# Optimization experiments

Hardware: AMD Instinct MI355X
Metric: run time of the kernel (lower is better)

The kernel has to match this reference:

```python
import jax, jax.numpy as jnp
import numpy as np

EPS = 1e-5


def layer_norm(x, g, b):
    mu = jnp.mean(x, axis=-1, keepdims=True)
    var = jnp.var(x, axis=-1, keepdims=True)
    return (x - mu) * jax.lax.rsqrt(var + EPS) * g + b


def setup_inputs() -> dict:
    key = jax.random.key(0)
    ks = jax.random.split(key, 10)
    B, N, D, H, DFF = 4, 2048, 384, 6, 2048
    s = lambda fan: 1.0 / np.sqrt(fan)
    return {
        "x": jax.random.normal(ks[0], (B, N, D), dtype=jnp.float32),
        "norm_g": jnp.ones((D,), jnp.float32),
        "norm_b": jnp.zeros((D,), jnp.float32),
        "w_qkv": jax.random.uniform(ks[1], (D, 3 * D), jnp.float32, -s(D), s(D)),
        "b_qkv": jax.random.uniform(ks[2], (3 * D,), jnp.float32, -s(D), s(D)),
        "w1": jax.random.uniform(ks[3], (D, DFF), jnp.float32, -s(D), s(D)),
        "b1": jax.random.uniform(ks[4], (DFF,), jnp.float32, -s(D), s(D)),
        "w2": jax.random.uniform(ks[5], (DFF, D), jnp.float32, -s(DFF), s(DFF)),
        "b2": jax.random.uniform(ks[6], (D,), jnp.float32, -s(DFF), s(DFF)),
    }


def reference(x, norm_g, norm_b, w_qkv, b_qkv, w1, b1, w2, b2):
    H = 6
    B, N, D = x.shape
    hd = D // H
    scale = hd ** -0.5

    # --- attention (pre-norm, shared LayerNorm params) ---
    out = layer_norm(x, norm_g, norm_b)
    qkv = out @ w_qkv + b_qkv                     # [B, N, 3D]
    q, k, v = jnp.split(qkv, 3, axis=-1)
    to_heads = lambda t: t.reshape(B, N, H, hd).transpose(0, 2, 1, 3)  # b h n d
    q, k, v = to_heads(q), to_heads(k), to_heads(v)
    scores = jnp.einsum('bhid,bhjd->bhij', q, k) * scale
    attn = jax.nn.softmax(scores, axis=-1)        # dropout is identity in eval
    att = jnp.einsum('bhij,bhjd->bhid', attn, v)  # [B, H, N, hd]
    att = att.transpose(0, 2, 1, 3).reshape(B, N, D)
    x2 = x + att

    # --- MLP (same shared LayerNorm) ---
    y = layer_norm(x2, norm_g, norm_b)
    h = jax.nn.gelu(y @ w1 + b1, approximate=False)  # torch F.gelu exact
    mlp = h @ w2 + b2
    return x2 + mlp
```

## Files before the change

kernel.cpp:

```cpp
#include <hip/hip_runtime.h>
#include <cstdint>
#include <cstddef>

#define DEV static __device__ __forceinline__

typedef __attribute__((ext_vector_type(8))) short short8;
typedef __attribute__((ext_vector_type(16))) float f32x16;
typedef __attribute__((ext_vector_type(4))) unsigned short u16x4;
typedef __attribute__((ext_vector_type(2))) unsigned short u16x2;

constexpr int kB = 4, kN = 2048, kD = 384, kH = 6, kDFF = 2048;
constexpr int kM = kB * kN;
constexpr int kBH = kB * kH;
constexpr float kQPre = 0.18033688011112042f;

DEV float exp2fast(float f) { return __builtin_amdgcn_exp2f(f); }

DEV unsigned short f2b(float f) {
  union { float fp; uint32_t u; } v; v.fp = f;
  return (unsigned short)((v.u + 0x7fffu + ((v.u >> 16) & 1u)) >> 16);
}

DEV void gload16(const unsigned short* g, unsigned short* l) {
  __builtin_amdgcn_global_load_lds(
      (const __attribute__((address_space(1))) unsigned int*)g,
      (__attribute__((address_space(3))) unsigned int*)l, 16, 0, 0);
}

DEV float gelu_fast(float x) {
  float t = exp2fast(x * (2.3022081f + 0.1029432f * x * x));
  return x - x * __builtin_amdgcn_rcpf(t + 1.0f);
}

__global__ __launch_bounds__(256) void k_pre(
    const float* __restrict__ wqkv, unsigned short* __restrict__ wqkvT,
    const float* __restrict__ w1,   unsigned short* __restrict__ w1T,
    const float* __restrict__ w2,   unsigned short* __restrict__ w2T,
    const float* __restrict__ x, const float* __restrict__ g,
    const float* __restrict__ bta, unsigned short* __restrict__ y) {
  const int tid = threadIdx.x;
  if (blockIdx.x >= 492) {
    int row  = (blockIdx.x - 492) * 4 + (tid >> 6);
    int lane = tid & 63;
    const float* xr = x + (size_t)row * kD;
    float4 a = *(const float4*)(xr + lane * 4);
    float2 c = *(const float2*)(xr + 256 + lane * 2);
    float s  = a.x + a.y + a.z + a.w + c.x + c.y;
    float ss = a.x*a.x + a.y*a.y + a.z*a.z + a.w*a.w + c.x*c.x + c.y*c.y;
#pragma unroll
    for (int m = 1; m < 64; m <<= 1) {
      s  += __shfl_xor(s,  m, 64);
      ss += __shfl_xor(ss, m, 64);
    }
    float mean = s * (1.0f / kD);
    float var  = ss * (1.0f / kD) - mean * mean;
    float r = rsqrtf(var + 1e-5f);
    float4 g4 = *(const float4*)(g + lane * 4);
    float2 g2 = *(const float2*)(g + 256 + lane * 2);
    float4 b4 = *(const float4*)(bta + lane * 4);
    float2 b2 = *(const float2*)(bta + 256 + lane * 2);
    unsigned short* yr = y + (size_t)row * kD;
    u16x4 o4;
    o4[0] = f2b((a.x - mean) * r * g4.x + b4.x);
    o4[1] = f2b((a.y - mean) * r * g4.y + b4.y);
    o4[2] = f2b((a.z - mean) * r * g4.z + b4.z);
    o4[3] = f2b((a.w - mean) * r * g4.w + b4.w);
    *(u16x4*)(yr + lane * 4) = o4;
    u16x2 o2;
    o2[0] = f2b((c.x - mean) * r * g2.x + b2.x);
    o2[1] = f2b((c.y - mean) * r * g2.y + b2.y);
    *(u16x2*)(yr + 256 + lane * 2) = o2;
    return;
  }
  __shared__ unsigned short t[64][66];
  int idx = blockIdx.x;
  const float* w; unsigned short* wT; int K, Nn, nbk;
  if (idx < 108)      { w = wqkv; wT = wqkvT; K = 384;  Nn = 1152; nbk = 6; }
  else if (idx < 300) { w = w1;   wT = w1T;   K = 384;  Nn = 2048; nbk = 6;  idx -= 108; }
  else                { w = w2;   wT = w2T;   K = 2048; Nn = 384;  nbk = 32; idx -= 300; }
  const int bk = idx % nbk, bn = idx / nbk;
  const int k0 = bk << 6, n0 = bn << 6;
  const int cl = tid & 63, rw = tid >> 6;
#pragma unroll
  for (int it = 0; it < 16; ++it) {
    int kk = it * 4 + rw;
    t[cl][kk] = f2b(w[(size_t)(k0 + kk) * Nn + n0 + cl]);
  }
  __syncthreads();
  const int kq = (tid & 15) << 2;
  const int nr = tid >> 4;
#pragma unroll
  for (int it = 0; it < 4; ++it) {
    int nn = it * 16 + nr;
    u16x4 v;
    v[0] = t[nn][kq]; v[1] = t[nn][kq + 1]; v[2] = t[nn][kq + 2]; v[3] = t[nn][kq + 3];
    *(u16x4*)&wT[(size_t)(n0 + nn) * K + k0 + kq] = v;
  }
}

__global__ __launch_bounds__(256) void k_layernorm(
    const float* __restrict__ x, const float* __restrict__ g,
    const float* __restrict__ bta, unsigned short* __restrict__ y) {
  int row  = blockIdx.x * 4 + (threadIdx.x >> 6);
  int lane = threadIdx.x & 63;
  const float* xr = x + (size_t)row * kD;
  float4 a = *(const float4*)(xr + lane * 4);
  float2 c = *(const float2*)(xr + 256 + lane * 2);
  float s  = a.x + a.y + a.z + a.w + c.x + c.y;
  float ss = a.x*a.x + a.y*a.y + a.z*a.z + a.w*a.w + c.x*c.x + c.y*c.y;
#pragma unroll
  for (int m = 1; m < 64; m <<= 1) {
    s  += __shfl_xor(s,  m, 64);
    ss += __shfl_xor(ss, m, 64);
  }
  float mean = s * (1.0f / kD);
  float var  = ss * (1.0f / kD) - mean * mean;
  float r = rsqrtf(var + 1e-5f);
  float4 g4 = *(const float4*)(g + lane * 4);
  float2 g2 = *(const float2*)(g + 256 + lane * 2);
  float4 b4 = *(const float4*)(bta + lane * 4);
  float2 b2 = *(const float2*)(bta + 256 + lane * 2);
  unsigned short* yr = y + (size_t)row * kD;
  u16x4 o4;
  o4[0] = f2b((a.x - mean) * r * g4.x + b4.x);
  o4[1] = f2b((a.y - mean) * r * g4.y + b4.y);
  o4[2] = f2b((a.z - mean) * r * g4.z + b4.z);
  o4[3] = f2b((a.w - mean) * r * g4.w + b4.w);
  *(u16x4*)(yr + lane * 4) = o4;
  u16x2 o2;
  o2[0] = f2b((c.x - mean) * r * g2.x + b2.x);
  o2[1] = f2b((c.y - mean) * r * g2.y + b2.y);
  *(u16x2*)(yr + 256 + lane * 2) = o2;
}

template <int MODE, int TM>
__global__ __launch_bounds__(256) void k_gemm(
    const unsigned short* __restrict__ A, const unsigned short* __restrict__ Bt,
    const float* __restrict__ bias, int K, int Nn, int nbm,
    unsigned short* __restrict__ oq, unsigned short* __restrict__ okk,
    unsigned short* __restrict__ ov, unsigned short* __restrict__ oh,
    const float* __restrict__ res, float* __restrict__ out) {
  constexpr int FI = (TM >= 64) ? TM / 64 : 1;
  constexpr int FJ = (TM >= 64) ? 2 : 1;
  __shared__ unsigned short lA[2][TM * 32];
  __shared__ unsigned short lB[2][128 * 32];
  const int tid = threadIdx.x, wid = tid >> 6, lane = tid & 63;
  const int bm = blockIdx.x % nbm, bn = blockIdx.x / nbm;
  const int m0 = bm * TM, n0 = bn * 128;
  const int wr = (TM >= 64) ? (wid >> 1) : 0;
  const int wc = (TM >= 64) ? (wid & 1) : wid;
  const int wmo = wr * (TM >> 1);
  const int wno = wc * (FJ * 32);
  const int l31 = lane & 31, lh = lane >> 5;
  const int gsw = (l31 >> 1) & 3;

  f32x16 acc[FI][FJ];
#pragma unroll
  for (int i = 0; i < FI; i++)
#pragma unroll
    for (int j = 0; j < FJ; j++)
#pragma unroll
      for (int r = 0; r < 16; r++) acc[i][j][r] = 0.f;

  const int srow = (lane >> 2);
  const int scc  = (lane & 3) << 3;

  auto stage = [&](int buf, int k0) {
    if constexpr (TM >= 64) {
#pragma unroll
      for (int p = 0; p < TM / 64; p++) {
        int row = ((wid + (p << 2)) << 4) + srow;
        int sl  = ((lane & 3) ^ ((row >> 1) & 3)) << 3;
        gload16(A + (size_t)(m0 + row) * K + k0 + sl, &lA[buf][(row << 5) + scc]);
      }
    } else {
      if (tid < TM * 4) {
        int row = tid >> 2;
        int sl  = ((tid & 3) ^ ((row >> 1) & 3)) << 3;
        gload16(A + (size_t)(m0 + row) * K + k0 + sl,
                &lA[buf][(row << 5) + ((tid & 3) << 3)]);
      }
    }
#pragma unroll
    for (int p = 0; p < 2; p++) {
      int row = ((wid + (p << 2)) << 4) + srow;
      int sl  = ((lane & 3) ^ ((row >> 1) & 3)) << 3;
      gload16(Bt + (size_t)(n0 + row) * K + k0 + sl, &lB[buf][(row << 5) + scc]);
    }
  };

  stage(0, 0);

  const int nkt = K >> 5;
  for (int kt = 0; kt < nkt; ++kt) {
    const int cur = kt & 1;
    __syncthreads();
    if (kt + 1 < nkt) stage(cur ^ 1, (kt + 1) << 5);
    short8 af[FI][2], bf[FJ][2];
#pragma unroll
    for (int i = 0; i < FI; i++)
#pragma unroll
      for (int ks = 0; ks < 2; ks++)
        af[i][ks] = *(const short8*)&lA[cur][(wmo + (i << 5) + l31) * 32 +
                                            ((((ks << 1) + lh) ^ gsw) << 3)];
#pragma unroll
    for (int j = 0; j < FJ; j++)
#pragma unroll
      for (int ks = 0; ks < 2; ks++)
        bf[j][ks] = *(const short8*)&lB[cur][(wno + (j << 5) + l31) * 32 +
                                            ((((ks << 1) + lh) ^ gsw) << 3)];
#pragma unroll
    for (int i = 0; i < FI; i++)
#pragma unroll
      for (int j = 0; j < FJ; j++)
#pragma unroll
        for (int ks = 0; ks < 2; ks++)
          acc[i][j] = __builtin_amdgcn_mfma_f32_32x32x16_bf16(af[i][ks], bf[j][ks],
                                                              acc[i][j], 0, 0, 0);
  }

#pragma unroll
  for (int i = 0; i < FI; i++) {
#pragma unroll
    for (int j = 0; j < FJ; j++) {
      int col = n0 + wno + (j << 5) + l31;
      float bv = bias[col];
#pragma unroll
      for (int reg = 0; reg < 16; ++reg) {
        int m = m0 + wmo + (i << 5) + (reg & 3) + ((reg >> 2) << 3) + (lh << 2);
        float cvl = acc[i][j][reg] + bv;
        if (MODE == 0) {
          int bI = m >> 11, nI = m & 2047;
          if (col < 384) {
            int hh = col >> 6, dd = col & 63;
            oq[(((size_t)bI * kH + hh) * kN + nI) * 64 + dd] = f2b(cvl * kQPre);
          } else if (col < 768) {
            int c2 = col - 384; int hh = c2 >> 6, dd = c2 & 63;
            okk[(((size_t)bI * kH + hh) * kN + nI) * 64 + dd] = f2b(cvl);
          } else {
            int c2 = col - 768; int hh = c2 >> 6, dd = c2 & 63;
            ov[(((size_t)bI * kH + hh) * 64 + dd) * kN + nI] = f2b(cvl);
          }
        } else if (MODE == 1) {
          oh[(size_t)m * kDFF + col] = f2b(gelu_fast(cvl));
        } else {
          size_t idx = (size_t)m * kD + col;
          out[idx] = res[idx] + cvl;
        }
      }
    }
  }
}

__global__ __launch_bounds__(256) void k_attn(
    const unsigned short* __restrict__ Q, const unsigned short* __restrict__ Kg,
    const unsigned short* __restrict__ Vt, const float* __restrict__ x,
    float* __restrict__ x2) {
  __shared__ unsigned short sh[4 * 4096];
  unsigned short* lK = sh;
  unsigned short* lV = sh + 8192;
  const int tid = threadIdx.x, wid = tid >> 6, lane = tid & 63;
  const int swz = (blockIdx.x & 7) * (gridDim.x >> 3) + (blockIdx.x >> 3);
  const int bh = swz >> 5, qt = swz & 31;
  const int b = bh / kH, h = bh - b * kH;
  const unsigned short* Qp = Q  + (size_t)bh * kN * 64;
  const unsigned short* Kp = Kg + (size_t)bh * kN * 64;
  const unsigned short* Vp = Vt + (size_t)bh * 64 * kN;
  const int l31 = lane & 31, lh = lane >> 5;
  const int qh = wid & 1, kvh = wid >> 1;
  const int q0 = qt * 64;
  const int rsw7 = l31 & 7;

  const int sr  = ((wid << 3) + (lane >> 3));
  const int scc = (lane & 7) << 3;

  short8 qb[4];
#pragma unroll
  for (int ks = 0; ks < 4; ++ks)
    qb[ks] = *(const short8*)(Qp + (size_t)(q0 + qh * 32 + l31) * 64 + ks * 16 + lh * 8);

  f32x16 o[2];
#pragma unroll
  for (int dt = 0; dt < 2; ++dt)
#pragma unroll
    for (int r = 0; r < 16; r++) o[dt][r] = 0.f;
  float l_r = 0.f;

  auto stage = [&](int buf, int t) {
#pragma unroll
    for (int p = 0; p < 2; p++) {
      int r = sr + (p << 5);
      int sl = ((lane & 7) ^ (r & 7)) << 3;
      gload16(Kp + (size_t)(t * 64 + r) * 64 + sl, &lK[buf * 4096 + (r << 6) + scc]);
      gload16(Vp + (size_t)r * kN + t * 64 + sl,   &lV[buf * 4096 + (r << 6) + scc]);
    }
  };

  stage(0, 0);

  constexpr int kNT = kN / 64;
  for (int t = 0; t < kNT; ++t) {
    const int cur = t & 1;
    __syncthreads();
    if (t + 1 < kNT) stage(cur ^ 1, t + 1);

    f32x16 s;
#pragma unroll
    for (int r = 0; r < 16; r++) s[r] = 0.f;
#pragma unroll
    for (int ks = 0; ks < 4; ++ks) {
      short8 kf = *(const short8*)&lK[cur * 4096 + ((kvh * 32 + l31) << 6) +
                                      ((((ks << 1) + lh) ^ rsw7) << 3)];
      s = __builtin_amdgcn_mfma_f32_32x32x16_bf16(kf, qb[ks], s, 0, 0, 0);
    }

    uint32_t Aw[4], Bw[4];
    float lsum = 0.f;
#pragma unroll
    for (int g = 0; g < 4; ++g) {
      float p0 = exp2fast(s[4 * g + 0]);
      float p1 = exp2fast(s[4 * g + 1]);
      float p2 = exp2fast(s[4 * g + 2]);
      float p3 = exp2fast(s[4 * g + 3]);
      lsum += (p0 + p1) + (p2 + p3);
      asm("v_cvt_pk_bf16_f32 %0, %1, %2" : "=v"(Aw[g]) : "v"(p0), "v"(p1));
      asm("v_cvt_pk_bf16_f32 %0, %1, %2" : "=v"(Bw[g]) : "v"(p2), "v"(p3));
    }
    l_r += lsum + __shfl_xor(lsum, 32, 64);

    short8 pb[2];
#pragma unroll
    for (int ks = 0; ks < 2; ++ks) {
      uint32_t cA = lh ? Aw[2 * ks + 1] : Aw[2 * ks];
      uint32_t cB = lh ? Bw[2 * ks + 1] : Bw[2 * ks];
      uint32_t dA = lh ? Aw[2 * ks] : Aw[2 * ks + 1];
      uint32_t dB = lh ? Bw[2 * ks] : Bw[2 * ks + 1];
      uint32_t sA = __shfl_xor(dA, 32, 64);
      uint32_t sB = __shfl_xor(dB, 32, 64);
      union { uint32_t u[4]; short8 s8; } bld;
      bld.u[0] = lh ? sA : cA;
      bld.u[1] = lh ? sB : cB;
      bld.u[2] = lh ? cA : sA;
      bld.u[3] = lh ? cB : sB;
      pb[ks] = bld.s8;
    }

#pragma unroll
    for (int dt = 0; dt < 2; ++dt) {
#pragma unroll
      for (int ks = 0; ks < 2; ++ks) {
        short8 va = *(const short8*)&lV[cur * 4096 + (((dt << 5) + l31) << 6) +
                        ((((kvh << 2) + (ks << 1) + lh) ^ rsw7) << 3)];
        o[dt] = __builtin_amdgcn_mfma_f32_32x32x16_bf16(va, pb[ks], o[dt], 0, 0, 0);
      }
    }
  }

  __syncthreads();
  float* fb = (float*)sh;
  float* lb = (float*)sh + 64 * 65;
  const int q = qh * 32 + l31;
  if (kvh == 1) {
#pragma unroll
    for (int dt = 0; dt < 2; ++dt)
#pragma unroll
      for (int reg = 0; reg < 16; ++reg) {
        int d = (dt << 5) + (reg & 3) + ((reg >> 2) << 3) + (lh << 2);
        fb[q * 65 + d] = o[dt][reg];
      }
    if (lh == 0) lb[q] = l_r;
  }
  __syncthreads();
  if (kvh == 0) {
#pragma unroll
    for (int dt = 0; dt < 2; ++dt)
#pragma unroll
      for (int reg = 0; reg < 16; ++reg) {
        int d = (dt << 5) + (reg & 3) + ((reg >> 2) << 3) + (lh << 2);
        fb[q * 65 + d] += o[dt][reg];
      }
    if (lh == 0) lb[q] += l_r;
  }
  __syncthreads();
  {
    int row = tid >> 2, dc = (tid & 3) << 4;
    float inv = __builtin_amdgcn_rcpf(lb[row]);
    size_t base = ((size_t)(b * kN + q0 + row)) * kD + h * 64 + dc;
#pragma unroll
    for (int i = 0; i < 16; i += 4) {
      float4 xv = *(const float4*)(x + base + i);
      float4 ov;
      ov.x = xv.x + fb[row * 65 + dc + i + 0] * inv;
      ov.y = xv.y + fb[row * 65 + dc + i + 1] * inv;
      ov.z = xv.z + fb[row * 65 + dc + i + 2] * inv;
      ov.w = xv.w + fb[row * 65 + dc + i + 3] * inv;
      *(float4*)(x2 + base + i) = ov;
    }
  }
}

extern "C" void kernel_launch(void* const* d_in, const int* in_sizes, int n_in,
                              void* d_out, int out_size, void* d_ws, size_t ws_size,
                              hipStream_t stream) {
  const float* x    = (const float*)d_in[0];
  const float* ng   = (const float*)d_in[1];
  const float* nb   = (const float*)d_in[2];
  const float* wqkv = (const float*)d_in[3];
  const float* bqkv = (const float*)d_in[4];
  const float* w1   = (const float*)d_in[5];
  const float* b1   = (const float*)d_in[6];
  const float* w2   = (const float*)d_in[7];
  const float* b2   = (const float*)d_in[8];
  float* out = (float*)d_out;

  char* p = (char*)d_ws;
  auto take = [&](size_t bytes) -> char* {
    char* r = p; p += (bytes + 255) & ~(size_t)255; return r;
  };
  unsigned short* y     = (unsigned short*)take((size_t)kM * kD * 2);
  unsigned short* wqkvT = (unsigned short*)take((size_t)3 * kD * kD * 2);
  unsigned short* w1T   = (unsigned short*)take((size_t)kDFF * kD * 2);
  unsigned short* w2T   = (unsigned short*)take((size_t)kD * kDFF * 2);
  unsigned short* Qw    = (unsigned short*)take((size_t)kM * kD * 2);
  unsigned short* Kw    = (unsigned short*)take((size_t)kM * kD * 2);
  unsigned short* Vtw   = (unsigned short*)take((size_t)kM * kD * 2);
  float*          x2    = (float*)take((size_t)kM * kD * 4);
  unsigned short* hbuf  = (unsigned short*)take((size_t)kM * kDFF * 2);

  k_pre<<<492 + kM / 4, 256, 0, stream>>>(wqkv, wqkvT, w1, w1T, w2, w2T,
                                          x, ng, nb, y);
  k_gemm<0, 64><<<128 * 9, 256, 0, stream>>>(y, wqkvT, bqkv, kD, 3 * kD, 128,
                                             Qw, Kw, Vtw, nullptr, nullptr, nullptr);
  k_attn<<<kBH * 32, 256, 0, stream>>>(Qw, Kw, Vtw, x, x2);
  k_layernorm<<<kM / 4, 256, 0, stream>>>(x2, ng, nb, y);
  k_gemm<1, 128><<<64 * 16, 256, 0, stream>>>(y, w1T, b1, kD, kDFF, 64,
                                              nullptr, nullptr, nullptr, hbuf, nullptr, nullptr);
  k_gemm<2, 32><<<256 * 3, 256, 0, stream>>>(hbuf, w2T, b2, kDFF, kD, 256,
                                             nullptr, nullptr, nullptr, nullptr, x2, out);
}
```

Baseline: 148.4 us.

## Deepen GEMM K-tile to 64 with 8-slot XOR swizzle and shrink MLP1 tile

The bf16 MFMA GEMM now stages 64-wide K slices instead of 32. It uses a new 8-way XOR LDS swizzle and a reworked staging loop in which every thread issues async global-to-LDS loads. This halves the number of K iterations and barriers and gives each wave four MFMAs per fragment per step. The first MLP GEMM moves from 128-row to 64-row tiles, doubling its block count, and each wave is fixed to one 32-row fragment. The trade-off is twice the LDS per buffer, plus less operand reuse in the MLP1 GEMM in exchange for more parallelism.

```diff
diff --git a/kernel.cpp b/kernel.cpp
--- a/kernel.cpp
+++ b/kernel.cpp
@@ -140,19 +140,19 @@
     unsigned short* __restrict__ oq, unsigned short* __restrict__ okk,
     unsigned short* __restrict__ ov, unsigned short* __restrict__ oh,
     const float* __restrict__ res, float* __restrict__ out) {
-  constexpr int FI = (TM >= 64) ? TM / 64 : 1;
+  constexpr int FI = 1;
   constexpr int FJ = (TM >= 64) ? 2 : 1;
-  __shared__ unsigned short lA[2][TM * 32];
-  __shared__ unsigned short lB[2][128 * 32];
+  __shared__ unsigned short lA[2][TM * 64];
+  __shared__ unsigned short lB[2][128 * 64];
   const int tid = threadIdx.x, wid = tid >> 6, lane = tid & 63;
   const int bm = blockIdx.x % nbm, bn = blockIdx.x / nbm;
   const int m0 = bm * TM, n0 = bn * 128;
   const int wr = (TM >= 64) ? (wid >> 1) : 0;
   const int wc = (TM >= 64) ? (wid & 1) : wid;
-  const int wmo = wr * (TM >> 1);
+  const int wmo = wr * 32;
   const int wno = wc * (FJ * 32);
   const int l31 = lane & 31, lh = lane >> 5;
-  const int gsw = (l31 >> 1) & 3;
+  const int rsw = l31 & 7;
 
   f32x16 acc[FI][FJ];
 #pragma unroll
@@ -162,59 +162,52 @@
 #pragma unroll
       for (int r = 0; r < 16; r++) acc[i][j][r] = 0.f;
 
-  const int srow = (lane >> 2);
-  const int scc  = (lane & 3) << 3;
+  const int srow = tid >> 3;
+  const int sslot = tid & 7;
 
   auto stage = [&](int buf, int k0) {
-    if constexpr (TM >= 64) {
-#pragma unroll
-      for (int p = 0; p < TM / 64; p++) {
-        int row = ((wid + (p << 2)) << 4) + srow;
-        int sl  = ((lane & 3) ^ ((row >> 1) & 3)) << 3;
-        gload16(A + (size_t)(m0 + row) * K + k0 + sl, &lA[buf][(row << 5) + scc]);
-      }
-    } else {
-      if (tid < TM * 4) {
-        int row = tid >> 2;
-        int sl  = ((tid & 3) ^ ((row >> 1) & 3)) << 3;
-        gload16(A + (size_t)(m0 + row) * K + k0 + sl,
-                &lA[buf][(row << 5) + ((tid & 3) << 3)]);
-      }
-    }
-#pragma unroll
-    for (int p = 0; p < 2; p++) {
-      int row = ((wid + (p << 2)) << 4) + srow;
-      int sl  = ((lane & 3) ^ ((row >> 1) & 3)) << 3;
-      gload16(Bt + (size_t)(n0 + row) * K + k0 + sl, &lB[buf][(row << 5) + scc]);
+#pragma unroll
+    for (int p = 0; p < 4; p++) {
+      int row = (p << 5) + srow;
+      int sl  = (sslot ^ (row & 7)) << 3;
+      gload16(Bt + (size_t)(n0 + row) * K + k0 + sl,
+              &lB[buf][(row << 6) + (sslot << 3)]);
+    }
+#pragma unroll
+    for (int p = 0; p < TM / 32; p++) {
+      int row = (p << 5) + srow;
+      int sl  = (sslot ^ (row & 7)) << 3;
+      gload16(A + (size_t)(m0 + row) * K + k0 + sl,
+              &lA[buf][(row << 6) + (sslot << 3)]);
     }
   };
 
   stage(0, 0);
 
-  const int nkt = K >> 5;
+  const int nkt = K >> 6;
   for (int kt = 0; kt < nkt; ++kt) {
     const int cur = kt & 1;
     __syncthreads();
-    if (kt + 1 < nkt) stage(cur ^ 1, (kt + 1) << 5);
-    short8 af[FI][2], bf[FJ][2];
+    if (kt + 1 < nkt) stage(cur ^ 1, (kt + 1) << 6);
+    short8 af[FI][4], bf[FJ][4];
 #pragma unroll
     for (int i = 0; i < FI; i++)
 #pragma unroll
-      for (int ks = 0; ks < 2; ks++)
-        af[i][ks] = *(const short8*)&lA[cur][(wmo + (i << 5) + l31) * 32 +
-                                            ((((ks << 1) + lh) ^ gsw) << 3)];
+      for (int ks = 0; ks < 4; ks++)
+        af[i][ks] = *(const short8*)&lA[cur][((wmo + (i << 5) + l31) << 6) +
+                                            ((((ks << 1) + lh) ^ rsw) << 3)];
 #pragma unroll
     for (int j = 0; j < FJ; j++)
 #pragma unroll
-      for (int ks = 0; ks < 2; ks++)
-        bf[j][ks] = *(const short8*)&lB[cur][(wno + (j << 5) + l31) * 32 +
-                                            ((((ks << 1) + lh) ^ gsw) << 3)];
+      for (int ks = 0; ks < 4; ks++)
+        bf[j][ks] = *(const short8*)&lB[cur][((wno + (j << 5) + l31) << 6) +
+                                            ((((ks << 1) + lh) ^ rsw) << 3)];
 #pragma unroll
     for (int i = 0; i < FI; i++)
 #pragma unroll
       for (int j = 0; j < FJ; j++)
 #pragma unroll
-        for (int ks = 0; ks < 2; ks++)
+        for (int ks = 0; ks < 4; ks++)
           acc[i][j] = __builtin_amdgcn_mfma_f32_32x32x16_bf16(af[i][ks], bf[j][ks],
                                                               acc[i][j], 0, 0, 0);
   }
@@ -433,7 +426,7 @@
                                              Qw, Kw, Vtw, nullptr, nullptr, nullptr);
   k_attn<<<kBH * 32, 256, 0, stream>>>(Qw, Kw, Vtw, x, x2);
   k_layernorm<<<kM / 4, 256, 0, stream>>>(x2, ng, nb, y);
-  k_gemm<1, 128><<<64 * 16, 256, 0, stream>>>(y, w1T, b1, kD, kDFF, 64,
+  k_gemm<1, 64><<<128 * 16, 256, 0, stream>>>(y, w1T, b1, kD, kDFF, 128,
                                               nullptr, nullptr, nullptr, hbuf, nullptr, nullptr);
   k_gemm<2, 32><<<256 * 3, 256, 0, stream>>>(hbuf, w2T, b2, kDFF, kD, 256,
                                              nullptr, nullptr, nullptr, nullptr, x2, out);
```

Measured after the change: 135.2 us. 1.1x faster.
